# Kernel tuning notes

Hardware: AMD Instinct MI355X
Metric: run time of the kernel (lower is better)

Reference implementation:

```python
import jax, jax.numpy as jnp
import numpy as np
import math

B, L, D = 4, 4096, 512
P, V = 128, 8  # n_phases, value_dim
PI = math.pi

def _lin(x, w, b):
    return x @ w + b

def _gelu(x):
    return jax.nn.gelu(x, approximate=False)  # torch default exact GELU

def setup_inputs() -> dict:
    key = jax.random.key(0)
    ks = iter(jax.random.split(key, 32))
    def rn(shape, scale=0.02):
        return (jax.random.normal(next(ks), shape, dtype=jnp.float32) * scale)
    inp = {
        'x': jax.random.normal(next(ks), (B, L, D), dtype=jnp.float32),
        'pos_phases': jax.random.normal(next(ks), (L, D), dtype=jnp.float32) * PI,
        'magnitude_scale': jnp.float32(5.0),
        'w_v': rn((D, D)), 'b_v': jnp.zeros((D,), jnp.float32),
        'w_o': rn((D, D)), 'b_o': jnp.zeros((D,), jnp.float32),
        'w_m': rn((D, D)), 'b_m': jnp.zeros((D,), jnp.float32),
        'w_q': rn((D, D)), 'b_q': jnp.zeros((D,), jnp.float32),
        'w_ke': rn((D, P)), 'b_ke': jnp.zeros((P,), jnp.float32),
        'w_ve': rn((D, V)), 'b_ve': jnp.zeros((V,), jnp.float32),
        'w_s1': rn((2 * D, D)), 'b_s1': jnp.zeros((D,), jnp.float32),
        'w_s2': rn((D, P)), 'b_s2': jnp.zeros((P,), jnp.float32),
        'w_g': rn((D, 1)), 'b_g': jnp.zeros((1,), jnp.float32),
        'w_kv': rn((V, D)), 'b_kv': jnp.zeros((D,), jnp.float32),
        'ln_g': jnp.ones((2 * D,), jnp.float32), 'ln_b': jnp.zeros((2 * D,), jnp.float32),
        'w_t1': rn((2 * D, 2 * D)), 'b_t1': jnp.zeros((2 * D,), jnp.float32),
        'w_t2': rn((2 * D, D)), 'b_t2': jnp.zeros((D,), jnp.float32),
    }
    return inp

def _forward(x, pos_phases, magnitude_scale, w_v, b_v, w_o, b_o, w_m, b_m,
             w_q, b_q, w_ke, b_ke, w_ve, b_ve, w_s1, b_s1, w_s2, b_s2,
             w_g, b_g, w_kv, b_kv, ln_g, ln_b, w_t1, b_t1, w_t2, b_t2):
    b, l, d = x.shape
    phi = pos_phases[:l]                               # [L,D]
    cos_phi, sin_phi = jnp.cos(phi), jnp.sin(phi)
    # --- positional phasor memory ---
    v1 = _lin(x, w_v, b_v)                             # [B,L,D]
    magnitude = jax.nn.sigmoid(_lin(x, w_m, b_m)) * jnp.abs(magnitude_scale)
    weighted_v1 = magnitude * v1
    mem1_cos = jnp.cumsum(weighted_v1 * cos_phi, axis=1)
    mem1_sin = jnp.cumsum(weighted_v1 * sin_phi, axis=1)
    sqrt_mag = jnp.sqrt(jnp.cumsum(magnitude, axis=1) + 1e-8)
    mem1_cos = mem1_cos / sqrt_mag
    mem1_sin = mem1_sin / sqrt_mag
    phi_query = phi + _lin(x, w_q, b_q)
    pos_ret = (mem1_cos * jnp.cos(phi_query) + mem1_sin * jnp.sin(phi_query)) / math.sqrt(d)
    pos_out = _lin(pos_ret, w_o, b_o)                  # [B,L,D]
    # --- key-value phasor memory ---
    query_phase = jnp.tanh(_lin(x, w_ke, b_ke)) * PI   # [B,L,P]
    values = _lin(x, w_ve, b_ve)                       # [B,L,V]
    store_gate = jax.nn.sigmoid(_lin(x, w_g, b_g))     # [B,L,1]
    positions = jnp.arange(1, l + 1, dtype=x.dtype)[None, :, None]
    context_avg = jnp.cumsum(x, axis=1) / positions
    sk = _lin(_gelu(_lin(jnp.concatenate([x, context_avg], axis=-1), w_s1, b_s1)), w_s2, b_s2)
    storage_phase = jnp.tanh(sk) * PI                  # [B,L,P]
    gv = values * store_gate                           # [B,L,V]
    kv_bound_cos = jnp.cos(storage_phase)[..., None] * gv[:, :, None, :]  # [B,L,P,V]
    kv_bound_sin = jnp.sin(storage_phase)[..., None] * gv[:, :, None, :]
    kv_mem_cos = jnp.cumsum(kv_bound_cos, axis=1)
    kv_mem_sin = jnp.cumsum(kv_bound_sin, axis=1)
    gate_cumsum = jnp.clip(jnp.cumsum(store_gate, axis=1), 1.0, None)     # [B,L,1]
    inv = 1.0 / jnp.sqrt(gate_cumsum)[..., None]
    kv_mem_cos = kv_mem_cos * inv
    kv_mem_sin = kv_mem_sin * inv
    kv_retrieved = (jnp.cos(query_phase)[..., None] * kv_mem_cos
                    + jnp.sin(query_phase)[..., None] * kv_mem_sin).sum(axis=2) / math.sqrt(P)
    kv_out = _lin(kv_retrieved, w_kv, b_kv)            # [B,L,D]
    # --- output projection (dropout = eval/identity) ---
    combined = jnp.concatenate([pos_out, kv_out], axis=-1)  # [B,L,2D]
    mu = combined.mean(axis=-1, keepdims=True)
    var = combined.var(axis=-1, keepdims=True)
    ln = (combined - mu) / jnp.sqrt(var + 1e-5) * ln_g + ln_b
    return x + _lin(_gelu(_lin(ln, w_t1, b_t1)), w_t2, b_t2)

def reference(x, pos_phases, magnitude_scale, w_v, b_v, w_o, b_o, w_m, b_m,
              w_q, b_q, w_ke, b_ke, w_ve, b_ve, w_s1, b_s1, w_s2, b_s2,
              w_g, b_g, w_kv, b_kv, ln_g, ln_b, w_t1, b_t1, w_t2, b_t2):
    return _forward(x, pos_phases, magnitude_scale, w_v, b_v, w_o, b_o, w_m, b_m,
                    w_q, b_q, w_ke, b_ke, w_ve, b_ve, w_s1, b_s1, w_s2, b_s2,
                    w_g, b_g, w_kv, b_kv, ln_g, ln_b, w_t1, b_t1, w_t2, b_t2)
```

## Files before the change

kernel.cpp:

```cpp
#include <hip/hip_runtime.h>
#include <math.h>

#define NTOK 16384
#define LSEQ 4096
#define BATCH 4
#define DDIM 512
#define PDIM 128
#define VDIM 8
#define PI_F 3.14159265358979323846f

#define NC2 64
#define CL2 64
#define NC3 128
#define CL3 32

#define VMQ_S 1536

typedef __attribute__((ext_vector_type(8))) short bfrag8;
typedef __attribute__((ext_vector_type(4))) float facc4;

__device__ __forceinline__ float sigmoid_(float v) { return 1.0f / (1.0f + expf(-v)); }
__device__ __forceinline__ float gelu_(float v) { return 0.5f * v * (1.0f + erff(v * 0.70710678118654752f)); }

__device__ __forceinline__ unsigned short f2bf(float f) {
    unsigned int u = __builtin_bit_cast(unsigned int, f);
    u += 0x7fffu + ((u >> 16) & 1u);
    return (unsigned short)(u >> 16);
}
__device__ __forceinline__ float bf2f(unsigned short h) {
    return __builtin_bit_cast(float, ((unsigned int)h) << 16);
}
__device__ __forceinline__ float bflo(unsigned int w) { return __builtin_bit_cast(float, w << 16); }
__device__ __forceinline__ float bfhi(unsigned int w) { return __builtin_bit_cast(float, w & 0xffff0000u); }

__device__ __forceinline__ void async16(const unsigned short* g, unsigned short* l) {
    __builtin_amdgcn_global_load_lds(
        (const __attribute__((address_space(1))) unsigned int*)g,
        (__attribute__((address_space(3))) unsigned int*)l, 16, 0, 0);
}

__global__ __launch_bounds__(256) void gemm_bf16(
    const unsigned short* __restrict__ A, int ldA,
    const unsigned short* __restrict__ Wt,
    const float* __restrict__ bias, int K,
    float* __restrict__ Cf, unsigned short* __restrict__ Cb, int ldC, int colOff,
    const float* __restrict__ res, int ldRes,
    int act)
{
    __shared__ unsigned short Asm[2][128 * 32];
    __shared__ unsigned short Bsm[2][128 * 32];
    const int tid = threadIdx.x;
    const int lane = tid & 63;
    const int wv = tid >> 6;
    const int wm = wv & 1, wn = wv >> 1;
    const int quad = lane >> 4, cc = lane & 15;
    const int row0 = blockIdx.y << 7;
    const int col0 = blockIdx.x << 7;

    facc4 acc[4][4];
#pragma unroll
    for (int i = 0; i < 4; ++i)
#pragma unroll
        for (int j = 0; j < 4; ++j) acc[i][j] = (facc4){0.f, 0.f, 0.f, 0.f};

    const int rquad = tid >> 2;
    const int kq = tid & 3;

    const unsigned short* ga0 = A + (size_t)(row0 + rquad) * ldA + kq * 8;
    const unsigned short* ga1 = ga0 + (size_t)64 * ldA;
    const unsigned short* gb0 = Wt + (size_t)(col0 + rquad) * K + kq * 8;
    const unsigned short* gb1 = gb0 + (size_t)64 * K;

    async16(ga0, &Asm[0][tid * 8]);
    async16(ga1, &Asm[0][(256 + tid) * 8]);
    async16(gb0, &Bsm[0][tid * 8]);
    async16(gb1, &Bsm[0][(256 + tid) * 8]);
    __syncthreads();

    const int nk = K >> 5;
    int cur = 0;
    for (int t = 0; t < nk; ++t) {
        if (t + 1 < nk) {
            const int off = (t + 1) << 5;
            async16(ga0 + off, &Asm[cur ^ 1][tid * 8]);
            async16(ga1 + off, &Asm[cur ^ 1][(256 + tid) * 8]);
            async16(gb0 + off, &Bsm[cur ^ 1][tid * 8]);
            async16(gb1 + off, &Bsm[cur ^ 1][(256 + tid) * 8]);
        }
        bfrag8 afr[4], bfr[4];
#pragma unroll
        for (int mt = 0; mt < 4; ++mt)
            afr[mt] = *(const bfrag8*)&Asm[cur][(wm * 64 + mt * 16 + cc) * 32 + quad * 8];
#pragma unroll
        for (int nt = 0; nt < 4; ++nt)
            bfr[nt] = *(const bfrag8*)&Bsm[cur][(wn * 64 + nt * 16 + cc) * 32 + quad * 8];
#pragma unroll
        for (int mt = 0; mt < 4; ++mt)
#pragma unroll
            for (int nt = 0; nt < 4; ++nt)
                acc[mt][nt] = __builtin_amdgcn_mfma_f32_16x16x32_bf16(
                    afr[mt], bfr[nt], acc[mt][nt], 0, 0, 0);
        __syncthreads();
        cur ^= 1;
    }

#pragma unroll
    for (int nt = 0; nt < 4; ++nt) {
        int col = col0 + wn * 64 + nt * 16 + cc;
        float bvv = bias[col];
#pragma unroll
        for (int mt = 0; mt < 4; ++mt) {
            int rowb = row0 + wm * 64 + mt * 16 + quad * 4;
#pragma unroll
            for (int r = 0; r < 4; ++r) {
                float v = acc[mt][nt][r] + bvv;
                if (act == 1) v = gelu_(v);
                size_t row = (size_t)(rowb + r);
                if (res) v += res[row * ldRes + col];
                size_t idx = row * ldC + colOff + col;
                if (Cf) Cf[idx] = v;
                else    Cb[idx] = f2bf(v);
            }
        }
    }
}

__global__ __launch_bounds__(256) void k_wcvt(const float* __restrict__ W, int K, int N,
                                              unsigned short* __restrict__ Wt)
{
    __shared__ float t[32][33];
    int bx = blockIdx.x, by = blockIdx.y;
    int tid = threadIdx.x;
    int tx = tid & 31, ty = tid >> 5;
#pragma unroll
    for (int r = 0; r < 4; ++r) {
        int k = by * 32 + ty + r * 8;
        t[ty + r * 8][tx] = W[(size_t)k * N + bx * 32 + tx];
    }
    __syncthreads();
#pragma unroll
    for (int r = 0; r < 4; ++r) {
        int n = bx * 32 + ty + r * 8;
        Wt[(size_t)n * K + by * 32 + tx] = f2bf(t[tx][ty + r * 8]);
    }
}

__global__ void k_xcvt(const float* __restrict__ x, unsigned short* __restrict__ xcat)
{
    int g = blockIdx.x * 256 + threadIdx.x;
    int c = g & 511, r = g >> 9;
    xcat[(size_t)r * 1024 + c] = f2bf(x[g]);
}

__global__ void k_bpack(const float* __restrict__ b0, const float* __restrict__ b1,
                        const float* __restrict__ b2, float* __restrict__ dst)
{
    int i = blockIdx.x * 256 + threadIdx.x;
    if (i < 512) dst[i] = b0[i];
    else if (i < 1024) dst[i] = b1[i - 512];
    else if (i < 1536) dst[i] = b2[i - 1024];
}

__global__ void k_phi(const float* __restrict__ pp, float* __restrict__ cphi,
                      float* __restrict__ sphi, int n)
{
    int i = blockIdx.x * 256 + threadIdx.x;
    if (i < n) {
        float s, c;
        sincosf(pp[i], &s, &c);
        cphi[i] = c;
        sphi[i] = s;
    }
}

__global__ __launch_bounds__(256) void k_glin(const float* __restrict__ x,
                                              const float* __restrict__ wg,
                                              const float* __restrict__ bg,
                                              float* __restrict__ glin)
{
    int wid = threadIdx.x >> 6, lane = threadIdx.x & 63;
    int row = blockIdx.x * 4 + wid;
    const float4* xr = (const float4*)(x + (size_t)row * DDIM);
    const float4* w4 = (const float4*)wg;
    float4 a0 = xr[lane], a1 = xr[lane + 64];
    float4 w0 = w4[lane], w1 = w4[lane + 64];
    float p = a0.x * w0.x + a0.y * w0.y + a0.z * w0.z + a0.w * w0.w
            + a1.x * w1.x + a1.y * w1.y + a1.z * w1.z + a1.w * w1.w;
    for (int d = 32; d >= 1; d >>= 1) p += __shfl_down(p, d, 64);
    if (lane == 0) glin[row] = p + bg[0];
}

__global__ __launch_bounds__(256) void k_values(const float* __restrict__ x,
                                                const float* __restrict__ wve,
                                                const float* __restrict__ bve,
                                                const float* __restrict__ glin,
                                                float* __restrict__ gv)
{
    int g = blockIdx.x * 256 + threadIdx.x;
    int m = g & 7, r = g >> 3;
    const float4* xr = (const float4*)(x + (size_t)r * DDIM);
    float acc = bve[m];
    for (int kq = 0; kq < 128; ++kq) {
        float4 a = xr[kq];
        int k = kq * 4;
        acc += a.x * wve[k * 8 + m] + a.y * wve[(k + 1) * 8 + m]
             + a.z * wve[(k + 2) * 8 + m] + a.w * wve[(k + 3) * 8 + m];
    }
    gv[g] = acc * sigmoid_(glin[r]);
}

__global__ __launch_bounds__(256) void k_scan1a(
    const unsigned short* __restrict__ vmq, const float* __restrict__ x,
    const float* __restrict__ cphi, const float* __restrict__ sphi,
    const float* __restrict__ msp, float* __restrict__ sum2)
{
    int g = blockIdx.x * 256 + threadIdx.x;
    int d = g & 511;
    int rest = g >> 9;
    int chunk = rest & (NC2 - 1);
    int b = rest >> 6;
    float msabs = fabsf(msp[0]);
    size_t row = (size_t)b * LSEQ + chunk * CL2;
    const unsigned short* vp = vmq + row * VMQ_S + d;
    const float* xp = x + row * DDIM + d;
    size_t pbase = ((size_t)chunk * CL2) * DDIM + d;
    float ac = 0.f, as = 0.f, am = 0.f, ax = 0.f;
    for (int i = 0; i < CL2; ++i) {
        float vv = bf2f(vp[0]);
        float ml = bf2f(vp[512]);
        float xv = xp[0];
        float cp = cphi[pbase], sp = sphi[pbase];
        float mag = msabs * sigmoid_(ml);
        float wv = mag * vv;
        ac += wv * cp; as += wv * sp; am += mag; ax += xv;
        vp += VMQ_S; xp += DDIM; pbase += DDIM;
    }
    int col = (b * DDIM + d) * NC2 + chunk;
    sum2[0 * 131072 + col] = ac;
    sum2[1 * 131072 + col] = as;
    sum2[2 * 131072 + col] = am;
    sum2[3 * 131072 + col] = ax;
}

__global__ __launch_bounds__(256) void k_scan1b(float* __restrict__ sum2)
{
    int g = blockIdx.x * 256 + threadIdx.x;
    float* p = sum2 + (size_t)g * NC2;
    float run = 0.f;
    for (int i = 0; i < NC2; ++i) { float t = p[i]; p[i] = run; run += t; }
}

__global__ __launch_bounds__(256) void k_scan1c(
    const unsigned short* __restrict__ vmq, const float* __restrict__ x,
    const float* __restrict__ cphi, const float* __restrict__ sphi,
    const float* __restrict__ msp, const float* __restrict__ sum2,
    unsigned short* __restrict__ pret, unsigned short* __restrict__ xcat)
{
    int g = blockIdx.x * 256 + threadIdx.x;
    int d = g & 511;
    int rest = g >> 9;
    int chunk = rest & (NC2 - 1);
    int b = rest >> 6;
    float msabs = fabsf(msp[0]);
    int col = (b * DDIM + d) * NC2 + chunk;
    float ac = sum2[col];
    float as = sum2[131072 + col];
    float am = sum2[2 * 131072 + col];
    float ax = sum2[3 * 131072 + col];
    size_t row = (size_t)b * LSEQ + chunk * CL2;
    const unsigned short* vp = vmq + row * VMQ_S + d;
    size_t base = row * DDIM + d;
    size_t pbase = ((size_t)chunk * CL2) * DDIM + d;
    int l = chunk * CL2;
    const float rsd = 0.04419417382415922f;
    for (int i = 0; i < CL2; ++i, ++l) {
        float vv = bf2f(vp[0]);
        float ml = bf2f(vp[512]);
        float q = bf2f(vp[1024]);
        float xv = x[base];
        float cp = cphi[pbase], sp = sphi[pbase];
        float mag = msabs * sigmoid_(ml);
        float wv = mag * vv;
        ac += wv * cp; as += wv * sp; am += mag; ax += xv;
        float inv = rsqrtf(am + 1e-8f);
        float mc = ac * inv, msn = as * inv;
        float cq, sq;
        sincosf(q, &sq, &cq);
        float cpq = cp * cq - sp * sq;
        float spq = sp * cq + cp * sq;
        pret[base] = f2bf((mc * cpq + msn * spq) * rsd);
        size_t orow = (size_t)b * LSEQ + l;
        xcat[orow * 1024 + 512 + d] = f2bf(ax / (float)(l + 1));
        vp += VMQ_S; base += DDIM; pbase += DDIM;
    }
}

__global__ void k_phases(const float* __restrict__ sk, const unsigned short* __restrict__ ke,
                         unsigned short* __restrict__ csp, unsigned short* __restrict__ ssp,
                         unsigned short* __restrict__ cqp, unsigned short* __restrict__ sqp, int n)
{
    int g = blockIdx.x * 256 + threadIdx.x;
    if (g < n) {
        float s, c;
        float spv = tanhf(sk[g]) * PI_F;
        sincosf(spv, &s, &c);
        csp[g] = f2bf(c); ssp[g] = f2bf(s);
        float qpv = tanhf(bf2f(ke[g])) * PI_F;
        sincosf(qpv, &s, &c);
        cqp[g] = f2bf(c); sqp[g] = f2bf(s);
    }
}

__global__ __launch_bounds__(1024) void k_gatescan(const float* __restrict__ glin,
                                                   float* __restrict__ gcum)
{
    __shared__ float s[1024];
    int b = blockIdx.x, tid = threadIdx.x;
    const float* gp = glin + (size_t)b * LSEQ + tid * 4;
    float e0 = sigmoid_(gp[0]);
    float e1 = sigmoid_(gp[1]);
    float e2 = sigmoid_(gp[2]);
    float e3 = sigmoid_(gp[3]);
    float l0 = e0, l1 = l0 + e1, l2 = l1 + e2, l3 = l2 + e3;
    s[tid] = l3;
    __syncthreads();
    for (int off = 1; off < 1024; off <<= 1) {
        float t = (tid >= off) ? s[tid - off] : 0.0f;
        __syncthreads();
        s[tid] += t;
        __syncthreads();
    }
    float excl = s[tid] - l3;
    float* out = gcum + (size_t)b * LSEQ + tid * 4;
    out[0] = excl + l0; out[1] = excl + l1; out[2] = excl + l2; out[3] = excl + l3;
}

__device__ __forceinline__ size_t kv_sum_idx(int b, int p, int v) {
    return ((((size_t)b * PDIM + p) * VDIM + v) * 2) * NC3;
}

__global__ __launch_bounds__(256) void k_kv1(const unsigned short* __restrict__ csp,
                                             const unsigned short* __restrict__ ssp,
                                             const float* __restrict__ gv,
                                             float* __restrict__ sum3)
{
    int blk = blockIdx.x;
    int chunk = blk & (NC3 - 1), b = blk >> 7;
    int tid = threadIdx.x;
    int w = tid >> 6, lane = tid & 63;
    int v = 2 * w + (lane & 1);
    int pq = lane >> 1;
    float sc[4] = {0, 0, 0, 0}, ss[4] = {0, 0, 0, 0};
    const uint2* c2p = (const uint2*)csp;
    const uint2* s2p = (const uint2*)ssp;
    int t = b * LSEQ + chunk * CL3;
    for (int i = 0; i < CL3; ++i, ++t) {
        uint2 cu = c2p[(size_t)t * 32 + pq];
        uint2 su = s2p[(size_t)t * 32 + pq];
        float g = gv[(size_t)t * VDIM + v];
        sc[0] += bflo(cu.x) * g; sc[1] += bfhi(cu.x) * g;
        sc[2] += bflo(cu.y) * g; sc[3] += bfhi(cu.y) * g;
        ss[0] += bflo(su.x) * g; ss[1] += bfhi(su.x) * g;
        ss[2] += bflo(su.y) * g; ss[3] += bfhi(su.y) * g;
    }
#pragma unroll
    for (int j = 0; j < 4; ++j) {
        size_t base = kv_sum_idx(b, pq * 4 + j, v) + chunk;
        sum3[base] = sc[j];
        sum3[base + NC3] = ss[j];
    }
}

__global__ __launch_bounds__(256) void k_kv2(float* __restrict__ sum3)
{
    int g = blockIdx.x * 256 + threadIdx.x;
    float* p = sum3 + (size_t)g * NC3;
    float run = 0.f;
    for (int i = 0; i < NC3; ++i) { float t = p[i]; p[i] = run; run += t; }
}

__global__ __launch_bounds__(256) void k_kv3(const unsigned short* __restrict__ csp,
                                             const unsigned short* __restrict__ ssp,
                                             const unsigned short* __restrict__ cqp,
                                             const unsigned short* __restrict__ sqp,
                                             const float* __restrict__ gv,
                                             const float* __restrict__ gcum,
                                             const float* __restrict__ sum3,
                                             float* __restrict__ kvr)
{
    int blk = blockIdx.x;
    int chunk = blk & (NC3 - 1), b = blk >> 7;
    int tid = threadIdx.x;
    int w = tid >> 6, lane = tid & 63;
    int v = 2 * w + (lane & 1);
    int pq = lane >> 1;
    float sc[4], ss[4];
#pragma unroll
    for (int j = 0; j < 4; ++j) {
        size_t base = kv_sum_idx(b, pq * 4 + j, v) + chunk;
        sc[j] = sum3[base];
        ss[j] = sum3[base + NC3];
    }
    const uint2* c2p = (const uint2*)csp;
    const uint2* s2p = (const uint2*)ssp;
    const uint2* cq2p = (const uint2*)cqp;
    const uint2* sq2p = (const uint2*)sqp;
    const float rsp = 0.08838834764831845f;
    int t = b * LSEQ + chunk * CL3;
    for (int i = 0; i < CL3; ++i, ++t) {
        uint2 cu = c2p[(size_t)t * 32 + pq];
        uint2 su = s2p[(size_t)t * 32 + pq];
        float g = gv[(size_t)t * VDIM + v];
        sc[0] += bflo(cu.x) * g; sc[1] += bfhi(cu.x) * g;
        sc[2] += bflo(cu.y) * g; sc[3] += bfhi(cu.y) * g;
        ss[0] += bflo(su.x) * g; ss[1] += bfhi(su.x) * g;
        ss[2] += bflo(su.y) * g; ss[3] += bfhi(su.y) * g;
        uint2 qcu = cq2p[(size_t)t * 32 + pq];
        uint2 qsu = sq2p[(size_t)t * 32 + pq];
        float part = bflo(qcu.x) * sc[0] + bfhi(qcu.x) * sc[1]
                   + bflo(qcu.y) * sc[2] + bfhi(qcu.y) * sc[3]
                   + bflo(qsu.x) * ss[0] + bfhi(qsu.x) * ss[1]
                   + bflo(qsu.y) * ss[2] + bfhi(qsu.y) * ss[3];
        part += __shfl_down(part, 32, 64);
        part += __shfl_down(part, 16, 64);
        part += __shfl_down(part, 8, 64);
        part += __shfl_down(part, 4, 64);
        part += __shfl_down(part, 2, 64);
        if (lane < 2) {
            float gc = gcum[t];
            float scale = rsqrtf(fmaxf(gc, 1.0f)) * rsp;
            kvr[(size_t)t * VDIM + v] = part * scale;
        }
    }
}

__global__ __launch_bounds__(256) void k_kvout(const float* __restrict__ kvr,
                                               const float* __restrict__ wkv,
                                               const float* __restrict__ bkv,
                                               unsigned short* __restrict__ comb)
{
    int g = blockIdx.x * 256 + threadIdx.x;
    int c = g & 511, r = g >> 9;
    const float* kr = kvr + (size_t)r * VDIM;
    float acc = bkv[c];
#pragma unroll
    for (int k = 0; k < 8; ++k) acc += kr[k] * wkv[k * DDIM + c];
    comb[(size_t)r * 1024 + 512 + c] = f2bf(acc);
}

__global__ __launch_bounds__(256) void k_ln(unsigned short* __restrict__ comb,
                                            const float* __restrict__ gam,
                                            const float* __restrict__ bet)
{
    int wid = threadIdx.x >> 6, lane = threadIdx.x & 63;
    int row = blockIdx.x * 4 + wid;
    unsigned int* rp = (unsigned int*)(comb + (size_t)row * 1024);
    uint4 u0 = *(uint4*)&rp[lane * 8];
    uint4 u1 = *(uint4*)&rp[lane * 8 + 4];
    unsigned int uu[8] = {u0.x, u0.y, u0.z, u0.w, u1.x, u1.y, u1.z, u1.w};
    float v[16];
    float s = 0.f, s2 = 0.f;
#pragma unroll
    for (int j = 0; j < 8; ++j) {
        v[2 * j] = bflo(uu[j]);
        v[2 * j + 1] = bfhi(uu[j]);
        s += v[2 * j] + v[2 * j + 1];
        s2 += v[2 * j] * v[2 * j] + v[2 * j + 1] * v[2 * j + 1];
    }
    for (int m = 32; m >= 1; m >>= 1) {
        s += __shfl_xor(s, m, 64);
        s2 += __shfl_xor(s2, m, 64);
    }
    float mu = s * (1.0f / 1024.0f);
    float var = s2 * (1.0f / 1024.0f) - mu * mu;
    float inv = rsqrtf(var + 1e-5f);
    int c0 = lane * 16;
    unsigned int ou[8];
#pragma unroll
    for (int j = 0; j < 8; ++j) {
        float g0 = gam[c0 + 2 * j], g1 = gam[c0 + 2 * j + 1];
        float b0 = bet[c0 + 2 * j], b1 = bet[c0 + 2 * j + 1];
        float o0 = (v[2 * j] - mu) * inv * g0 + b0;
        float o1 = (v[2 * j + 1] - mu) * inv * g1 + b1;
        ou[j] = (unsigned int)f2bf(o0) | ((unsigned int)f2bf(o1) << 16);
    }
    *(uint4*)&rp[lane * 8] = make_uint4(ou[0], ou[1], ou[2], ou[3]);
    *(uint4*)&rp[lane * 8 + 4] = make_uint4(ou[4], ou[5], ou[6], ou[7]);
}

extern "C" void kernel_launch(void* const* d_in, const int* in_sizes, int n_in,
                              void* d_out, int out_size, void* d_ws, size_t ws_size,
                              hipStream_t stream)
{
    const float* x    = (const float*)d_in[0];
    const float* pp   = (const float*)d_in[1];
    const float* msp  = (const float*)d_in[2];
    const float* w_v  = (const float*)d_in[3];
    const float* b_v  = (const float*)d_in[4];
    const float* w_o  = (const float*)d_in[5];
    const float* b_o  = (const float*)d_in[6];
    const float* w_m  = (const float*)d_in[7];
    const float* b_m  = (const float*)d_in[8];
    const float* w_q  = (const float*)d_in[9];
    const float* b_q  = (const float*)d_in[10];
    const float* w_ke = (const float*)d_in[11];
    const float* b_ke = (const float*)d_in[12];
    const float* w_ve = (const float*)d_in[13];
    const float* b_ve = (const float*)d_in[14];
    const float* w_s1 = (const float*)d_in[15];
    const float* b_s1 = (const float*)d_in[16];
    const float* w_s2 = (const float*)d_in[17];
    const float* b_s2 = (const float*)d_in[18];
    const float* w_g  = (const float*)d_in[19];
    const float* b_g  = (const float*)d_in[20];
    const float* w_kv = (const float*)d_in[21];
    const float* b_kv = (const float*)d_in[22];
    const float* ln_g = (const float*)d_in[23];
    const float* ln_b = (const float*)d_in[24];
    const float* w_t1 = (const float*)d_in[25];
    const float* b_t1 = (const float*)d_in[26];
    const float* w_t2 = (const float*)d_in[27];
    const float* b_t2 = (const float*)d_in[28];
    float* out = (float*)d_out;
    float* ws = (float*)d_ws;
    (void)ws_size; (void)n_in; (void)in_sizes; (void)out_size;

    unsigned short* VMQ    = (unsigned short*)(ws);
    float*          SKf    = ws + 4194304;
    unsigned short* CSP    = (unsigned short*)(ws + 8388608);
    unsigned short* SSP    = CSP + 2097152;
    unsigned short* CQP    = CSP + 2 * 2097152;
    unsigned short* SQP    = CSP + 3 * 2097152;
    unsigned short* KEbf   = (unsigned short*)(ws + 12582912);
    float* GVb   = ws + 13631488;
    float* GLINb = ws + 13762560;
    float* GCUMb = ws + 13778944;
    float* SUM2b = ws + 13795328;
    float* CBIAS = SUM2b;
    float* SUM3b = ws + 14319616;
    float* KVRb  = ws + 15368192;
    float* CPHIb = ws + 15499264;
    float* SPHIb = ws + 17596416;
    unsigned short* HSbf   = (unsigned short*)(ws + 15499264);
    unsigned short* PRETbf = (unsigned short*)(ws + 19693568);
    unsigned short* XCAT   = (unsigned short*)(ws + 23887872);
    unsigned short* COMBbf = XCAT;
    unsigned short* HTbf   = (unsigned short*)(ws);
    unsigned short* WT     = (unsigned short*)(ws + 32276480);
    unsigned short* wv_t  = WT;
    unsigned short* wm_t  = WT + 262144;
    unsigned short* wq_t  = WT + 524288;
    unsigned short* wo_t  = WT + 786432;
    unsigned short* wke_t = WT + 1048576;
    unsigned short* ws1_t = WT + 1114112;
    unsigned short* ws2_t = WT + 1638400;
    unsigned short* wt1_t = WT + 1703936;
    unsigned short* wt2_t = WT + 2752512;

    k_phi<<<8192, 256, 0, stream>>>(pp, CPHIb, SPHIb, 2097152);
    k_xcvt<<<32768, 256, 0, stream>>>(x, XCAT);
    k_wcvt<<<dim3(16, 16), 256, 0, stream>>>(w_v, 512, 512, wv_t);
    k_wcvt<<<dim3(16, 16), 256, 0, stream>>>(w_m, 512, 512, wm_t);
    k_wcvt<<<dim3(16, 16), 256, 0, stream>>>(w_q, 512, 512, wq_t);
    k_wcvt<<<dim3(16, 16), 256, 0, stream>>>(w_o, 512, 512, wo_t);
    k_wcvt<<<dim3(4, 16), 256, 0, stream>>>(w_ke, 512, 128, wke_t);
    k_wcvt<<<dim3(16, 32), 256, 0, stream>>>(w_s1, 1024, 512, ws1_t);
    k_wcvt<<<dim3(4, 16), 256, 0, stream>>>(w_s2, 512, 128, ws2_t);
    k_wcvt<<<dim3(32, 32), 256, 0, stream>>>(w_t1, 1024, 1024, wt1_t);
    k_wcvt<<<dim3(16, 32), 256, 0, stream>>>(w_t2, 1024, 512, wt2_t);
    k_bpack<<<6, 256, 0, stream>>>(b_v, b_m, b_q, CBIAS);

    gemm_bf16<<<dim3(12, 128), 256, 0, stream>>>(XCAT, 1024, wv_t, CBIAS, 512, nullptr, VMQ, VMQ_S, 0, nullptr, 0, 0);
    gemm_bf16<<<dim3(1, 128), 256, 0, stream>>>(XCAT, 1024, wke_t, b_ke, 512, nullptr, KEbf, 128, 0, nullptr, 0, 0);
    k_glin<<<4096, 256, 0, stream>>>(x, w_g, b_g, GLINb);
    k_values<<<512, 256, 0, stream>>>(x, w_ve, b_ve, GLINb, GVb);

    k_scan1a<<<512, 256, 0, stream>>>(VMQ, x, CPHIb, SPHIb, msp, SUM2b);
    k_scan1b<<<32, 256, 0, stream>>>(SUM2b);
    k_scan1c<<<512, 256, 0, stream>>>(VMQ, x, CPHIb, SPHIb, msp, SUM2b, PRETbf, XCAT);

    gemm_bf16<<<dim3(4, 128), 256, 0, stream>>>(XCAT, 1024, ws1_t, b_s1, 1024, nullptr, HSbf, 512, 0, nullptr, 0, 1);
    gemm_bf16<<<dim3(1, 128), 256, 0, stream>>>(HSbf, 512, ws2_t, b_s2, 512, SKf, nullptr, 128, 0, nullptr, 0, 0);

    k_phases<<<8192, 256, 0, stream>>>(SKf, KEbf, CSP, SSP, CQP, SQP, 2097152);
    k_gatescan<<<4, 1024, 0, stream>>>(GLINb, GCUMb);

    k_kv1<<<512, 256, 0, stream>>>(CSP, SSP, GVb, SUM3b);
    k_kv2<<<32, 256, 0, stream>>>(SUM3b);
    k_kv3<<<512, 256, 0, stream>>>(CSP, SSP, CQP, SQP, GVb, GCUMb, SUM3b, KVRb);

    gemm_bf16<<<dim3(4, 128), 256, 0, stream>>>(PRETbf, 512, wo_t, b_o, 512, nullptr, COMBbf, 1024, 0, nullptr, 0, 0);
    k_kvout<<<32768, 256, 0, stream>>>(KVRb, w_kv, b_kv, COMBbf);
    k_ln<<<4096, 256, 0, stream>>>(COMBbf, ln_g, ln_b);
    gemm_bf16<<<dim3(8, 128), 256, 0, stream>>>(COMBbf, 1024, wt1_t, b_t1, 1024, nullptr, HTbf, 1024, 0, nullptr, 0, 1);
    gemm_bf16<<<dim3(4, 128), 256, 0, stream>>>(HTbf, 1024, wt2_t, b_t2, 1024, out, nullptr, 512, 0, x, 512, 0);
}
```

Before: 648.3 us.

## Triple-buffer GEMM LDS loads with explicit vmcnt waits and XCD-aware block swizzle

The bf16 GEMM's LDS staging goes from double to triple buffering, so tile t+2 is prefetched while tile t is computed. Full syncthreads are replaced by explicit s_waitcnt vmcnt counts and raw barriers. Block indices are also remapped so consecutive row-blocks land on the same XCD, aiming for better L2 reuse of A/W tiles. This costs more LDS per block, which may lower occupancy, and depends on hand-computed waitcnt values being correct and on grid dimensions dividing by 8.

```diff
diff --git a/kernel.cpp b/kernel.cpp
--- a/kernel.cpp
+++ b/kernel.cpp
@@ -47,15 +47,22 @@
     const float* __restrict__ res, int ldRes,
     int act)
 {
-    __shared__ unsigned short Asm[2][128 * 32];
-    __shared__ unsigned short Bsm[2][128 * 32];
+    __shared__ unsigned short Asm[3][128 * 32];
+    __shared__ unsigned short Bsm[3][128 * 32];
     const int tid = threadIdx.x;
     const int lane = tid & 63;
     const int wv = tid >> 6;
     const int wm = wv & 1, wn = wv >> 1;
     const int quad = lane >> 4, cc = lane & 15;
-    const int row0 = blockIdx.y << 7;
-    const int col0 = blockIdx.x << 7;
+
+    const int C = gridDim.x, R = gridDim.y;
+    const int bid = blockIdx.x + C * blockIdx.y;
+    const int xcd = bid & 7;
+    const int s = bid >> 3;
+    const int by = xcd * (R >> 3) + s / C;
+    const int bx = s - (s / C) * C;
+    const int row0 = by << 7;
+    const int col0 = bx << 7;
 
     facc4 acc[4][4];
 #pragma unroll
@@ -71,22 +78,28 @@
     const unsigned short* gb0 = Wt + (size_t)(col0 + rquad) * K + kq * 8;
     const unsigned short* gb1 = gb0 + (size_t)64 * K;
 
-    async16(ga0, &Asm[0][tid * 8]);
-    async16(ga1, &Asm[0][(256 + tid) * 8]);
-    async16(gb0, &Bsm[0][tid * 8]);
-    async16(gb1, &Bsm[0][(256 + tid) * 8]);
-    __syncthreads();
-
     const int nk = K >> 5;
+
+    auto stage = [&](int t, int buf) {
+        const int off = t << 5;
+        async16(ga0 + off, &Asm[buf][tid * 8]);
+        async16(ga1 + off, &Asm[buf][(256 + tid) * 8]);
+        async16(gb0 + off, &Bsm[buf][tid * 8]);
+        async16(gb1 + off, &Bsm[buf][(256 + tid) * 8]);
+    };
+
+    stage(0, 0);
+    stage(1, 1);
+
     int cur = 0;
     for (int t = 0; t < nk; ++t) {
-        if (t + 1 < nk) {
-            const int off = (t + 1) << 5;
-            async16(ga0 + off, &Asm[cur ^ 1][tid * 8]);
-            async16(ga1 + off, &Asm[cur ^ 1][(256 + tid) * 8]);
-            async16(gb0 + off, &Bsm[cur ^ 1][tid * 8]);
-            async16(gb1 + off, &Bsm[cur ^ 1][(256 + tid) * 8]);
-        }
+        int nb = cur + 2; if (nb >= 3) nb -= 3;
+        if (t + 2 < nk) stage(t + 2, nb);
+        if (t + 2 < nk)      asm volatile("s_waitcnt vmcnt(8)" ::: "memory");
+        else if (t + 1 < nk) asm volatile("s_waitcnt vmcnt(4)" ::: "memory");
+        else                 asm volatile("s_waitcnt vmcnt(0)" ::: "memory");
+        __builtin_amdgcn_s_barrier();
+        __builtin_amdgcn_sched_barrier(0);
         bfrag8 afr[4], bfr[4];
 #pragma unroll
         for (int mt = 0; mt < 4; ++mt)
@@ -100,8 +113,9 @@
             for (int nt = 0; nt < 4; ++nt)
                 acc[mt][nt] = __builtin_amdgcn_mfma_f32_16x16x32_bf16(
                     afr[mt], bfr[nt], acc[mt][nt], 0, 0, 0);
-        __syncthreads();
-        cur ^= 1;
+        asm volatile("s_waitcnt lgkmcnt(0)" ::: "memory");
+        __builtin_amdgcn_s_barrier();
+        cur = cur + 1; if (cur >= 3) cur -= 3;
     }
 
 #pragma unroll
```

After: 623.6 us. 3.8% less time.
